# Optimization experiments

Hardware: AMD Instinct MI355X
Metric: run time of the kernel (lower is better)

## Reference

```python
import jax, jax.numpy as jnp
import numpy as np

NUM_HEADS = 8
EPS = 1e-5


def setup_inputs() -> dict:
    key = jax.random.key(0)
    ks = jax.random.split(key, 12)
    B, S, D = 16384, 12, 512
    s = 1.0 / np.sqrt(D)
    return {
        "x": jax.random.normal(ks[0], (B, S, D), dtype=jnp.float32),
        "Wq": jax.random.uniform(ks[1], (D, D), jnp.float32, -s, s),
        "bq": jax.random.uniform(ks[2], (D,), jnp.float32, -s, s),
        "Wk": jax.random.uniform(ks[3], (D, D), jnp.float32, -s, s),
        "bk": jax.random.uniform(ks[4], (D,), jnp.float32, -s, s),
        "Wv": jax.random.uniform(ks[5], (D, D), jnp.float32, -s, s),
        "bv": jax.random.uniform(ks[6], (D,), jnp.float32, -s, s),
        "adj_bias": jnp.zeros((NUM_HEADS, S, S), dtype=jnp.float32),
        "Wo": jax.random.uniform(ks[7], (D, D), jnp.float32, -s, s),
        "bo": jax.random.uniform(ks[8], (D,), jnp.float32, -s, s),
        "gamma": jnp.ones((D,), dtype=jnp.float32),
        "beta": jnp.zeros((D,), dtype=jnp.float32),
    }


def reference(x, Wq, bq, Wk, bk, Wv, bv, adj_bias, Wo, bo, gamma, beta):
    B, S, D = x.shape
    H = NUM_HEADS
    hd = D // H
    # QKV projections -> (B, H, S, hd)
    def proj(W, b):
        return (jnp.einsum('bsd,de->bse', x, W) + b).reshape(B, S, H, hd).transpose(0, 2, 1, 3)
    q = proj(Wq, bq)
    k = proj(Wk, bk)
    v = proj(Wv, bv)
    # scores with learned adjacency bias: (B, H, S, S)
    scores = jnp.einsum('bhsd,bhtd->bhst', q, k) / np.sqrt(hd).astype(np.float32)
    scores = scores + adj_bias[None, :, :S, :S]
    attn = jax.nn.softmax(scores, axis=-1)  # dropout is identity in eval mode
    out = jnp.einsum('bhst,bhtd->bhsd', attn, v)
    out = out.transpose(0, 2, 1, 3).reshape(B, S, D)
    out = jnp.einsum('bsd,de->bse', out, Wo) + bo
    # residual (in_dim == out_dim) + LayerNorm
    y = out + x
    mu = jnp.mean(y, axis=-1, keepdims=True)
    var = jnp.mean(jnp.square(y - mu), axis=-1, keepdims=True)
    return (y - mu) * jax.lax.rsqrt(var + EPS) * gamma + beta
```

## Files before the change

### kernel.cpp

```cpp
#include <hip/hip_runtime.h>
#include <hip/hip_bf16.h>

#define D_DIM 512
#define S_LEN 12
#define H_NUM 8
#define WMAT 262144

#define G_B1 8
#define ROWS1 96
#define THREADS1 768
#define QS 72
#define VS 102
#define X_OFF   0
#define Q_OFF   98304
#define K_OFF   112128
#define V_OFF   125952
#define P_OFF   139008
#define SMEM1   146688

#define G_B2 8
#define ROWS2 96
#define THREADS2 1024
#define AST_OFF 0
#define RED_OFF 98304
#define MU_OFF  110976
#define SMEM2   111744

typedef __attribute__((ext_vector_type(8))) short bf16x8;
typedef __attribute__((ext_vector_type(4))) float f32x4;

__device__ __forceinline__ unsigned short f2bf(float f) {
    union { float f; unsigned u; } c; c.f = f;
    unsigned r = c.u + 0x7fffu + ((c.u >> 16) & 1u);
    return (unsigned short)(r >> 16);
}
__device__ __forceinline__ float bf2f(unsigned short u) {
    union { unsigned u; float f; } c; c.u = ((unsigned)u) << 16;
    return c.f;
}
__device__ __forceinline__ int xswc(int row, int col) {
    return row * 512 + (((col >> 3) ^ (row & 7)) << 3) + (col & 7);
}
__device__ __forceinline__ int qsw72(int row, int col) {
    return row * QS + (((col >> 3) ^ (row & 7)) << 3) + (col & 7);
}

__global__ void prep_weights(const float* __restrict__ Wq, const float* __restrict__ Wk,
                             const float* __restrict__ Wv, const float* __restrict__ Wo,
                             unsigned short* __restrict__ wt) {
    int idx = blockIdx.x * 256 + threadIdx.x;
    int mat = idx >> 18;
    int rem = idx & (WMAT - 1);
    int e = rem >> 9, d = rem & 511;
    const float* W = (mat == 0) ? Wq : (mat == 1) ? Wk : (mat == 2) ? Wv : Wo;
    wt[idx] = f2bf(W[d * D_DIM + e]);
}

__global__ __launch_bounds__(THREADS1, 3) void qkv_attn(
    const float* __restrict__ x, const unsigned short* __restrict__ wt,
    const float* __restrict__ bq, const float* __restrict__ bk, const float* __restrict__ bv,
    const float* __restrict__ adj, float* __restrict__ aout)
{
    extern __shared__ char smem[];
    unsigned short* Xh = (unsigned short*)(smem + X_OFF);
    unsigned short* Qh = (unsigned short*)(smem + Q_OFF);
    unsigned short* Kh = (unsigned short*)(smem + K_OFF);
    unsigned short* Vt = (unsigned short*)(smem + V_OFF);
    float* Pl = (float*)(smem + P_OFF);

    const int tid  = threadIdx.x;
    const int lane = tid & 63;
    const int w    = tid >> 6;
    const int lr   = lane & 15;
    const int lg   = lane >> 4;
    const int lr12 = (lr < 12) ? lr : 11;
    const size_t row0 = (size_t)blockIdx.x * ROWS1;

    #pragma unroll
    for (int it = 0; it < 16; ++it) {
        int idx = it * THREADS1 + tid;
        int r = idx >> 7, col = (idx & 127) << 2;
        float4 v = *(const float4*)(x + (row0 + r) * (size_t)D_DIM + col);
        ushort4 pk;
        pk.x = f2bf(v.x); pk.y = f2bf(v.y); pk.z = f2bf(v.z); pk.w = f2bf(v.w);
        *(ushort4*)(Xh + xswc(r, col)) = pk;
    }
    __syncthreads();

    const int mat  = w >> 2;
    const int colt = w & 3;
    const int colh = colt * 16 + lr;
    const float* bsel = (mat == 0) ? bq : (mat == 1) ? bk : bv;
    const int rb = w * S_LEN;

    #pragma unroll 1
    for (int h = 0; h < H_NUM; ++h) {
        f32x4 acc[6];
        #pragma unroll
        for (int mt = 0; mt < 6; ++mt) acc[mt] = (f32x4){0.f, 0.f, 0.f, 0.f};

        const unsigned short* bAp = wt + (size_t)mat * WMAT + (h * 64 + colh) * D_DIM + lg * 8;
        bf16x8 bc = *(const bf16x8*)(bAp);
        #pragma unroll
        for (int ks = 0; ks < 16; ++ks) {
            bf16x8 bn;
            if (ks < 15) bn = *(const bf16x8*)(bAp + (ks + 1) * 32);
            #pragma unroll
            for (int mt = 0; mt < 6; ++mt) {
                bf16x8 af = *(const bf16x8*)(Xh + xswc(mt * 16 + lr, ks * 32 + lg * 8));
                acc[mt] = __builtin_amdgcn_mfma_f32_16x16x32_bf16(af, bc, acc[mt], 0, 0, 0);
            }
            if (ks < 15) bc = bn;
        }
        {
            float bias = bsel[h * 64 + colh];
            if (mat == 2) {
                #pragma unroll
                for (int mt = 0; mt < 6; ++mt) {
                    int rbase = mt * 16 + lg * 4;
                    ushort2 p0, p1;
                    p0.x = f2bf(acc[mt][0] + bias); p0.y = f2bf(acc[mt][1] + bias);
                    p1.x = f2bf(acc[mt][2] + bias); p1.y = f2bf(acc[mt][3] + bias);
                    *(ushort2*)(Vt + colh * VS + rbase)     = p0;
                    *(ushort2*)(Vt + colh * VS + rbase + 2) = p1;
                }
            } else {
                unsigned short* T = (mat == 0) ? Qh : Kh;
                #pragma unroll
                for (int mt = 0; mt < 6; ++mt)
                    #pragma unroll
                    for (int j = 0; j < 4; ++j)
                        T[qsw72(mt * 16 + lg * 4 + j, colh)] = f2bf(acc[mt][j] + bias);
            }
        }
        __syncthreads();

        if (w < 8) {
            f32x4 sacc = (f32x4){0.f, 0.f, 0.f, 0.f};
            #pragma unroll
            for (int k2 = 0; k2 < 2; ++k2) {
                bf16x8 ak = *(const bf16x8*)(Kh + qsw72(rb + lr12, k2 * 32 + lg * 8));
                bf16x8 aq = *(const bf16x8*)(Qh + qsw72(rb + lr12, k2 * 32 + lg * 8));
                sacc = __builtin_amdgcn_mfma_f32_16x16x32_bf16(ak, aq, sacc, 0, 0, 0);
            }
            float ab4[4] = {0.f, 0.f, 0.f, 0.f};
            if (lg < 3 && lr < 12) {
                float4 t4 = *(const float4*)(adj + (h * S_LEN + lr) * S_LEN + lg * 4);
                ab4[0] = t4.x; ab4[1] = t4.y; ab4[2] = t4.z; ab4[3] = t4.w;
            }
            float sc[4], e4[4];
            float m = -1e30f;
            #pragma unroll
            for (int j = 0; j < 4; ++j) {
                int t = lg * 4 + j;
                sc[j] = (t < 12) ? (sacc[j] * 0.125f + ab4[j]) : -1e30f;
                m = fmaxf(m, sc[j]);
            }
            m = fmaxf(m, __shfl_xor(m, 16));
            m = fmaxf(m, __shfl_xor(m, 32));
            float ssum = 0.f;
            #pragma unroll
            for (int j = 0; j < 4; ++j) { e4[j] = __expf(sc[j] - m); ssum += e4[j]; }
            ssum += __shfl_xor(ssum, 16);
            ssum += __shfl_xor(ssum, 32);
            float inv = 1.f / ssum;
            float* Pw = Pl + w * 240;
            if (lr < 12 && lg < 3) {
                f32x4 pvec = (f32x4){e4[0] * inv, e4[1] * inv, e4[2] * inv, e4[3] * inv};
                *(f32x4*)(Pw + lr * 20 + lg * 4) = pvec;
            }
            float vv[12];
            #pragma unroll
            for (int t = 0; t < 12; ++t) vv[t] = bf2f(Vt[lane * VS + rb + t]);
            #pragma unroll
            for (int ss = 0; ss < 12; ++ss) {
                f32x4 pa = *(const f32x4*)(Pw + ss * 20);
                f32x4 pb = *(const f32x4*)(Pw + ss * 20 + 4);
                f32x4 pc = *(const f32x4*)(Pw + ss * 20 + 8);
                float o = 0.f;
                #pragma unroll
                for (int t = 0; t < 4; ++t) o += pa[t] * vv[t];
                #pragma unroll
                for (int t = 0; t < 4; ++t) o += pb[t] * vv[4 + t];
                #pragma unroll
                for (int t = 0; t < 4; ++t) o += pc[t] * vv[8 + t];
                aout[(row0 + rb + ss) * (size_t)D_DIM + h * 64 + lane] = o;
            }
        }
        __syncthreads();
    }
}

__global__ __launch_bounds__(THREADS2) void oproj_ln(
    const float* __restrict__ x, const unsigned short* __restrict__ wt,
    const float* __restrict__ bo, const float* __restrict__ gamma,
    const float* __restrict__ beta, float* __restrict__ out)
{
    extern __shared__ char smem[];
    unsigned short* Ast = (unsigned short*)(smem + AST_OFF);
    float* red   = (float*)(smem + RED_OFF);
    float* musig = (float*)(smem + MU_OFF);

    const int tid  = threadIdx.x;
    const int lane = tid & 63;
    const int w    = tid >> 6;
    const int lr   = lane & 15;
    const int lg   = lane >> 4;
    const size_t row0 = (size_t)blockIdx.x * ROWS2;

    #pragma unroll
    for (int it = 0; it < 12; ++it) {
        int idx = it * THREADS2 + tid;
        int r = idx >> 7, col = (idx & 127) << 2;
        float4 v = *(const float4*)(out + (row0 + r) * (size_t)D_DIM + col);
        ushort4 pk;
        pk.x = f2bf(v.x); pk.y = f2bf(v.y); pk.z = f2bf(v.z); pk.w = f2bf(v.w);
        *(ushort4*)(Ast + xswc(r, col)) = pk;
    }
    __syncthreads();

    f32x4 Y[6][2];
    #pragma unroll
    for (int mt = 0; mt < 6; ++mt)
        #pragma unroll
        for (int nt = 0; nt < 2; ++nt) Y[mt][nt] = (f32x4){0.f, 0.f, 0.f, 0.f};

    const unsigned short* obase = wt + (size_t)3 * WMAT + (w * 32 + lr) * D_DIM;
    #pragma unroll 2
    for (int ks = 0; ks < 16; ++ks) {
        bf16x8 afr[6];
        #pragma unroll
        for (int mt = 0; mt < 6; ++mt)
            afr[mt] = *(const bf16x8*)(Ast + xswc(mt * 16 + lr, ks * 32 + lg * 8));
        #pragma unroll
        for (int nt = 0; nt < 2; ++nt) {
            bf16x8 bfr = *(const bf16x8*)(obase + nt * 16 * D_DIM + ks * 32 + lg * 8);
            #pragma unroll
            for (int mt = 0; mt < 6; ++mt)
                Y[mt][nt] = __builtin_amdgcn_mfma_f32_16x16x32_bf16(afr[mt], bfr, Y[mt][nt], 0, 0, 0);
        }
    }

    float bo2[2], gm2[2], bt2[2];
    int cols[2];
    #pragma unroll
    for (int nt = 0; nt < 2; ++nt) {
        cols[nt] = w * 32 + nt * 16 + lr;
        bo2[nt] = bo[cols[nt]]; gm2[nt] = gamma[cols[nt]]; bt2[nt] = beta[cols[nt]];
    }
    #pragma unroll
    for (int mt = 0; mt < 6; ++mt)
        #pragma unroll
        for (int j = 0; j < 4; ++j) {
            int rowl = mt * 16 + lg * 4 + j;
            const float* xrow = x + (row0 + rowl) * (size_t)D_DIM;
            float ps = 0.f, pq = 0.f;
            #pragma unroll
            for (int nt = 0; nt < 2; ++nt) {
                float y = Y[mt][nt][j] + bo2[nt] + xrow[cols[nt]];
                Y[mt][nt][j] = y;
                ps += y; pq += y * y;
            }
            ps += __shfl_xor(ps, 1); pq += __shfl_xor(pq, 1);
            ps += __shfl_xor(ps, 2); pq += __shfl_xor(pq, 2);
            ps += __shfl_xor(ps, 4); pq += __shfl_xor(pq, 4);
            ps += __shfl_xor(ps, 8); pq += __shfl_xor(pq, 8);
            if (lr == 0) { red[rowl * 33 + w * 2] = ps; red[rowl * 33 + w * 2 + 1] = pq; }
        }
    __syncthreads();
    if (tid < ROWS2) {
        float s = 0.f, q = 0.f;
        #pragma unroll
        for (int w16 = 0; w16 < 16; ++w16) { s += red[tid * 33 + w16 * 2]; q += red[tid * 33 + w16 * 2 + 1]; }
        float mu = s * (1.f / 512.f);
        float var = q * (1.f / 512.f) - mu * mu;
        musig[tid * 2] = mu;
        musig[tid * 2 + 1] = rsqrtf(var + 1e-5f);
    }
    __syncthreads();
    #pragma unroll
    for (int mt = 0; mt < 6; ++mt)
        #pragma unroll
        for (int j = 0; j < 4; ++j) {
            int rowl = mt * 16 + lg * 4 + j;
            float mu = musig[rowl * 2], rs = musig[rowl * 2 + 1];
            float* orow = out + (row0 + rowl) * (size_t)D_DIM;
            #pragma unroll
            for (int nt = 0; nt < 2; ++nt)
                orow[cols[nt]] = (Y[mt][nt][j] - mu) * rs * gm2[nt] + bt2[nt];
        }
}

extern "C" void kernel_launch(void* const* d_in, const int* in_sizes, int n_in,
                              void* d_out, int out_size, void* d_ws, size_t ws_size,
                              hipStream_t stream) {
    (void)in_sizes; (void)n_in; (void)out_size; (void)ws_size;
    const float* x     = (const float*)d_in[0];
    const float* Wq    = (const float*)d_in[1];
    const float* bq    = (const float*)d_in[2];
    const float* Wk    = (const float*)d_in[3];
    const float* bk    = (const float*)d_in[4];
    const float* Wv    = (const float*)d_in[5];
    const float* bv    = (const float*)d_in[6];
    const float* adj   = (const float*)d_in[7];
    const float* Wo    = (const float*)d_in[8];
    const float* bo    = (const float*)d_in[9];
    const float* gamma = (const float*)d_in[10];
    const float* beta  = (const float*)d_in[11];
    unsigned short* wt = (unsigned short*)d_ws;
    float* outf = (float*)d_out;

    prep_weights<<<4096, 256, 0, stream>>>(Wq, Wk, Wv, Wo, wt);
    qkv_attn<<<16384 / G_B1, THREADS1, SMEM1, stream>>>(x, wt, bq, bk, bv, adj, outf);
    oproj_ln<<<16384 / G_B2, THREADS2, SMEM2, stream>>>(x, wt, bo, gamma, beta, outf);
}
```

Baseline: 1.113 ms.

## Restructure QKV-attention kernel to process four heads per pass with 3x3 MFMA tiles

The QKV+attention kernel now handles 48 rows (4 sequences) per block with 1024 threads and computes four heads per pass, so only two passes are needed instead of eight. Each wave computes a 3x3 grid of MFMA tiles, reusing A and B fragments across tiles rather than a 6x1 strip, and all 16 waves then take part in the attention stage. V is stored row-major with the same swizzle as Q and K. This cuts barriers and raises register reuse, but the per-block X tile is smaller, so the weights are re-read from global memory twice as often, and the larger register footprint may lower occupancy.

```diff
diff --git a/kernel.cpp b/kernel.cpp
--- a/kernel.cpp
+++ b/kernel.cpp
@@ -6,17 +6,17 @@
 #define H_NUM 8
 #define WMAT 262144
 
-#define G_B1 8
-#define ROWS1 96
-#define THREADS1 768
+#define G_B1 4
+#define ROWS1 48
+#define THREADS1 1024
 #define QS 72
-#define VS 102
+#define HBLK 3456
 #define X_OFF   0
-#define Q_OFF   98304
-#define K_OFF   112128
-#define V_OFF   125952
-#define P_OFF   139008
-#define SMEM1   146688
+#define Q_OFF   49152
+#define K_OFF   76800
+#define V_OFF   104448
+#define P_OFF   132096
+#define SMEM1   147456
 
 #define G_B2 8
 #define ROWS2 96
@@ -56,7 +56,7 @@
     wt[idx] = f2bf(W[d * D_DIM + e]);
 }
 
-__global__ __launch_bounds__(THREADS1, 3) void qkv_attn(
+__global__ __launch_bounds__(THREADS1) void qkv_attn(
     const float* __restrict__ x, const unsigned short* __restrict__ wt,
     const float* __restrict__ bq, const float* __restrict__ bk, const float* __restrict__ bv,
     const float* __restrict__ adj, float* __restrict__ aout)
@@ -65,7 +65,7 @@
     unsigned short* Xh = (unsigned short*)(smem + X_OFF);
     unsigned short* Qh = (unsigned short*)(smem + Q_OFF);
     unsigned short* Kh = (unsigned short*)(smem + K_OFF);
-    unsigned short* Vt = (unsigned short*)(smem + V_OFF);
+    unsigned short* Vh = (unsigned short*)(smem + V_OFF);
     float* Pl = (float*)(smem + P_OFF);
 
     const int tid  = threadIdx.x;
@@ -77,7 +77,7 @@
     const size_t row0 = (size_t)blockIdx.x * ROWS1;
 
     #pragma unroll
-    for (int it = 0; it < 16; ++it) {
+    for (int it = 0; it < 6; ++it) {
         int idx = it * THREADS1 + tid;
         int r = idx >> 7, col = (idx & 127) << 2;
         float4 v = *(const float4*)(x + (row0 + r) * (size_t)D_DIM + col);
@@ -87,60 +87,81 @@
     }
     __syncthreads();
 
-    const int mat  = w >> 2;
-    const int colt = w & 3;
-    const int colh = colt * 16 + lr;
-    const float* bsel = (mat == 0) ? bq : (mat == 1) ? bk : bv;
-    const int rb = w * S_LEN;
+    int matn[3], hhn[3], c0n[3];
+    #pragma unroll
+    for (int nt = 0; nt < 3; ++nt) {
+        int colglob = w * 48 + nt * 16;
+        matn[nt] = colglob >> 8;
+        int rem = colglob & 255;
+        hhn[nt] = rem >> 6;
+        c0n[nt] = rem & 63;
+    }
+    const int ab = w & 3;
+    const int ah = w >> 2;
+    const int rbA = ab * S_LEN;
 
     #pragma unroll 1
-    for (int h = 0; h < H_NUM; ++h) {
-        f32x4 acc[6];
-        #pragma unroll
-        for (int mt = 0; mt < 6; ++mt) acc[mt] = (f32x4){0.f, 0.f, 0.f, 0.f};
-
-        const unsigned short* bAp = wt + (size_t)mat * WMAT + (h * 64 + colh) * D_DIM + lg * 8;
-        bf16x8 bc = *(const bf16x8*)(bAp);
+    for (int hg = 0; hg < 2; ++hg) {
+        f32x4 acc[3][3];
+        #pragma unroll
+        for (int mt = 0; mt < 3; ++mt)
+            #pragma unroll
+            for (int nt = 0; nt < 3; ++nt) acc[mt][nt] = (f32x4){0.f, 0.f, 0.f, 0.f};
+
+        const unsigned short* bp[3];
+        bf16x8 bc[3];
+        #pragma unroll
+        for (int nt = 0; nt < 3; ++nt) {
+            bp[nt] = wt + (size_t)matn[nt] * WMAT +
+                     ((hg * 4 + hhn[nt]) * 64 + c0n[nt] + lr) * D_DIM + lg * 8;
+            bc[nt] = *(const bf16x8*)bp[nt];
+        }
         #pragma unroll
         for (int ks = 0; ks < 16; ++ks) {
-            bf16x8 bn;
-            if (ks < 15) bn = *(const bf16x8*)(bAp + (ks + 1) * 32);
-            #pragma unroll
-            for (int mt = 0; mt < 6; ++mt) {
-                bf16x8 af = *(const bf16x8*)(Xh + xswc(mt * 16 + lr, ks * 32 + lg * 8));
-                acc[mt] = __builtin_amdgcn_mfma_f32_16x16x32_bf16(af, bc, acc[mt], 0, 0, 0);
-            }
-            if (ks < 15) bc = bn;
-        }
+            bf16x8 bn[3];
+            if (ks < 15) {
+                #pragma unroll
+                for (int nt = 0; nt < 3; ++nt)
+                    bn[nt] = *(const bf16x8*)(bp[nt] + (ks + 1) * 32);
+            }
+            bf16x8 af[3];
+            #pragma unroll
+            for (int mt = 0; mt < 3; ++mt)
+                af[mt] = *(const bf16x8*)(Xh + xswc(mt * 16 + lr, ks * 32 + lg * 8));
+            #pragma unroll
+            for (int nt = 0; nt < 3; ++nt)
+                #pragma unroll
+                for (int mt = 0; mt < 3; ++mt)
+                    acc[mt][nt] = __builtin_amdgcn_mfma_f32_16x16x32_bf16(af[mt], bc[nt], acc[mt][nt], 0, 0, 0);
+            if (ks < 15) {
+                #pragma unroll
+                for (int nt = 0; nt < 3; ++nt) bc[nt] = bn[nt];
+            }
+        }
+        #pragma unroll
+        for (int nt = 0; nt < 3; ++nt) {
+            int mat = matn[nt];
+            unsigned short* T = ((mat == 0) ? Qh : (mat == 1) ? Kh : Vh) + hhn[nt] * HBLK;
+            const float* bsel = (mat == 0) ? bq : (mat == 1) ? bk : bv;
+            float bias = bsel[(hg * 4 + hhn[nt]) * 64 + c0n[nt] + lr];
+            #pragma unroll
+            for (int mt = 0; mt < 3; ++mt)
+                #pragma unroll
+                for (int j = 0; j < 4; ++j)
+                    T[qsw72(mt * 16 + lg * 4 + j, c0n[nt] + lr)] = f2bf(acc[mt][nt][j] + bias);
+        }
+        __syncthreads();
+
         {
-            float bias = bsel[h * 64 + colh];
-            if (mat == 2) {
-                #pragma unroll
-                for (int mt = 0; mt < 6; ++mt) {
-                    int rbase = mt * 16 + lg * 4;
-                    ushort2 p0, p1;
-                    p0.x = f2bf(acc[mt][0] + bias); p0.y = f2bf(acc[mt][1] + bias);
-                    p1.x = f2bf(acc[mt][2] + bias); p1.y = f2bf(acc[mt][3] + bias);
-                    *(ushort2*)(Vt + colh * VS + rbase)     = p0;
-                    *(ushort2*)(Vt + colh * VS + rbase + 2) = p1;
-                }
-            } else {
-                unsigned short* T = (mat == 0) ? Qh : Kh;
-                #pragma unroll
-                for (int mt = 0; mt < 6; ++mt)
-                    #pragma unroll
-                    for (int j = 0; j < 4; ++j)
-                        T[qsw72(mt * 16 + lg * 4 + j, colh)] = f2bf(acc[mt][j] + bias);
-            }
-        }
-        __syncthreads();
-
-        if (w < 8) {
+            const int h = hg * 4 + ah;
+            const unsigned short* Qb = Qh + ah * HBLK;
+            const unsigned short* Kb = Kh + ah * HBLK;
+            const unsigned short* Vb = Vh + ah * HBLK;
             f32x4 sacc = (f32x4){0.f, 0.f, 0.f, 0.f};
             #pragma unroll
             for (int k2 = 0; k2 < 2; ++k2) {
-                bf16x8 ak = *(const bf16x8*)(Kh + qsw72(rb + lr12, k2 * 32 + lg * 8));
-                bf16x8 aq = *(const bf16x8*)(Qh + qsw72(rb + lr12, k2 * 32 + lg * 8));
+                bf16x8 ak = *(const bf16x8*)(Kb + qsw72(rbA + lr12, k2 * 32 + lg * 8));
+                bf16x8 aq = *(const bf16x8*)(Qb + qsw72(rbA + lr12, k2 * 32 + lg * 8));
                 sacc = __builtin_amdgcn_mfma_f32_16x16x32_bf16(ak, aq, sacc, 0, 0, 0);
             }
             float ab4[4] = {0.f, 0.f, 0.f, 0.f};
@@ -171,7 +192,7 @@
             }
             float vv[12];
             #pragma unroll
-            for (int t = 0; t < 12; ++t) vv[t] = bf2f(Vt[lane * VS + rb + t]);
+            for (int t = 0; t < 12; ++t) vv[t] = bf2f(Vb[qsw72(rbA + t, lane)]);
             #pragma unroll
             for (int ss = 0; ss < 12; ++ss) {
                 f32x4 pa = *(const f32x4*)(Pw + ss * 20);
@@ -184,10 +205,10 @@
                 for (int t = 0; t < 4; ++t) o += pb[t] * vv[4 + t];
                 #pragma unroll
                 for (int t = 0; t < 4; ++t) o += pc[t] * vv[8 + t];
-                aout[(row0 + rb + ss) * (size_t)D_DIM + h * 64 + lane] = o;
-            }
-        }
-        __syncthreads();
+                aout[(row0 + rbA + ss) * (size_t)D_DIM + h * 64 + lane] = o;
+            }
+        }
+        if (hg == 0) __syncthreads();
     }
 }
 
```

After: 1.713 ms. 53.9% more time.
